# Kernel tuning notes

Measured on AMD Instinct MI355X. Metric: run time of the kernel, lower is better.

## Reference

```python
import jax, jax.numpy as jnp
import numpy as np
import math

B, S, D, H = 2, 2048, 1024, 16
DK = D // H


def setup_inputs() -> dict:
    key = jax.random.key(0)
    k1, k2, k3, k4, k5, k6 = jax.random.split(key, 6)
    scale = 1.0 / math.sqrt(D)
    return {
        "query": jax.random.normal(k1, (B, S, D), dtype=jnp.float32),
        "key": jax.random.normal(k2, (B, S, D), dtype=jnp.float32),
        "value": jax.random.normal(k3, (B, S, D), dtype=jnp.float32),
        "Wqkv": jax.random.normal(k4, (D, D), dtype=jnp.float32) * scale,
        "Wout": jax.random.normal(k5, (D, D), dtype=jnp.float32) * scale,
        "mask": jax.random.randint(k6, (B, 1, S, S), 0, 2, dtype=jnp.int32),
    }


def reference(query, key, value, Wqkv, Wout, mask):
    # Single shared QKV projection (same weight applied to q, k, v), no bias.
    q = query @ Wqkv.T
    k = key @ Wqkv.T
    v = value @ Wqkv.T
    # Faithful to the original: reshape (B, S, D) -> (B, H, S, DK) directly
    # (torch .reshape(n_batches, h, -1, d_k), NOT view+transpose).
    q = q.reshape(B, H, S, DK)
    k = k.reshape(B, H, S, DK)
    v = v.reshape(B, H, S, DK)
    scores = jnp.einsum("bhqd,bhkd->bhqk", q, k) / math.sqrt(DK)
    scores = jnp.where(mask == 0, jnp.float32(-1e9), scores)
    p_attn = jax.nn.softmax(scores, axis=-1)  # dropout is identity in eval
    x = jnp.einsum("bhqk,bhkd->bhqd", p_attn, v)  # [B,H,S,DK]
    x = x.transpose(0, 2, 1, 3).reshape(B, S, H * DK)
    return x @ Wout.T
```

## Files before the change

### kernel.cpp

```cpp
#include <hip/hip_runtime.h>
#include <stdint.h>


typedef __bf16 bf16;
typedef __bf16 bf16x8 __attribute__((ext_vector_type(8)));
typedef __bf16 bf16x4 __attribute__((ext_vector_type(4)));
typedef float f32x4 __attribute__((ext_vector_type(4)));

#define MFMA16(a, b, c) __builtin_amdgcn_mfma_f32_16x16x32_bf16((a), (b), (c), 0, 0, 0)
#define EXP2(x) __builtin_amdgcn_exp2f(x)

static constexpr int BATCH = 2;
static constexpr int SEQ = 2048;
static constexpr int DIM = 1024;
static constexpr int DK = 64;
static constexpr float QSCALE = 0.125f * 1.44269504088896340736f;

template <typename T>
struct Stripe;
template <>
struct Stripe<bf16> {
  uint4 v;
};
template <>
struct Stripe<float> {
  float4 a, b;
};

__device__ inline Stripe<bf16> load_stripe(const bf16* p) {
  Stripe<bf16> s;
  s.v = *(const uint4*)p;
  return s;
}
__device__ inline Stripe<float> load_stripe(const float* p) {
  Stripe<float> s;
  s.a = *(const float4*)p;
  s.b = *(const float4*)(p + 4);
  return s;
}
__device__ inline void store_stripe(bf16* d, const Stripe<bf16>& s) { *(uint4*)d = s.v; }
__device__ inline void store_stripe(bf16* d, const Stripe<float>& s) {
  bf16x8 v;
  v[0] = (bf16)s.a.x;
  v[1] = (bf16)s.a.y;
  v[2] = (bf16)s.a.z;
  v[3] = (bf16)s.a.w;
  v[4] = (bf16)s.b.x;
  v[5] = (bf16)s.b.y;
  v[6] = (bf16)s.b.z;
  v[7] = (bf16)s.b.w;
  *(bf16x8*)d = v;
}

__global__ __launch_bounds__(256) void mask_bits_kernel(const int* __restrict__ mask,
                                                        unsigned long long* __restrict__ bits) {
  int idx = blockIdx.x * 256 + threadIdx.x;
  int m = mask[idx];
  unsigned long long bal = __ballot(m != 0);
  if ((threadIdx.x & 63) == 0) bits[idx >> 6] = bal;
}

template <typename TA, typename TW, typename TC>
__global__ __launch_bounds__(256, 2) void gemm_bt(const TA* __restrict__ A0,
                                                  const TA* __restrict__ A1,
                                                  const TA* __restrict__ A2,
                                                  const TW* __restrict__ W,
                                                  TC* __restrict__ C0,
                                                  TC* __restrict__ C1,
                                                  TC* __restrict__ C2,
                                                  float scale0) {
  constexpr int K = 1024, N = 1024, LDA = 40;
  __shared__ bf16 As[128 * LDA];
  __shared__ bf16 Bs[128 * LDA];

  const TA* A = (blockIdx.z == 0) ? A0 : (blockIdx.z == 1) ? A1 : A2;
  TC* C = (blockIdx.z == 0) ? C0 : (blockIdx.z == 1) ? C1 : C2;
  const float sc = (blockIdx.z == 0) ? scale0 : 1.0f;

  const int tid = threadIdx.x;
  const int lane = tid & 63;
  const int wv = tid >> 6;
  const int wm = wv >> 1, wn = wv & 1;
  const int lrow = lane & 15, quad = lane >> 4;
  const int m0 = blockIdx.y * 128, n0 = blockIdx.x * 128;

  const f32x4 fz = {0.f, 0.f, 0.f, 0.f};
  f32x4 acc[4][4];
#pragma unroll
  for (int i = 0; i < 4; ++i)
#pragma unroll
    for (int j = 0; j < 4; ++j) acc[i][j] = fz;

  const int r0 = tid >> 2;
  const int c0 = (tid & 3) * 8;
  const TA* pa0 = A + (size_t)(m0 + r0) * K + c0;
  const TA* pa1 = A + (size_t)(m0 + r0 + 64) * K + c0;
  const TW* pb0 = W + (size_t)(n0 + r0) * K + c0;
  const TW* pb1 = W + (size_t)(n0 + r0 + 64) * K + c0;
  bf16* wa0 = &As[r0 * LDA + c0];
  bf16* wa1 = &As[(r0 + 64) * LDA + c0];
  bf16* wb0 = &Bs[r0 * LDA + c0];
  bf16* wb1 = &Bs[(r0 + 64) * LDA + c0];

  Stripe<TA> ra0 = load_stripe(pa0);
  Stripe<TA> ra1 = load_stripe(pa1);
  Stripe<TW> rb0 = load_stripe(pb0);
  Stripe<TW> rb1 = load_stripe(pb1);

  for (int k0 = 0; k0 < K; k0 += 32) {
    __syncthreads();
    store_stripe(wa0, ra0);
    store_stripe(wa1, ra1);
    store_stripe(wb0, rb0);
    store_stripe(wb1, rb1);
    __syncthreads();
    if (k0 + 32 < K) {
      ra0 = load_stripe(pa0 + k0 + 32);
      ra1 = load_stripe(pa1 + k0 + 32);
      rb0 = load_stripe(pb0 + k0 + 32);
      rb1 = load_stripe(pb1 + k0 + 32);
    }
    bf16x8 af[4], bfr[4];
#pragma unroll
    for (int mt = 0; mt < 4; ++mt)
      af[mt] = *(const bf16x8*)(&As[(wm * 64 + mt * 16 + lrow) * LDA + quad * 8]);
#pragma unroll
    for (int nt = 0; nt < 4; ++nt)
      bfr[nt] = *(const bf16x8*)(&Bs[(wn * 64 + nt * 16 + lrow) * LDA + quad * 8]);
#pragma unroll
    for (int mt = 0; mt < 4; ++mt)
#pragma unroll
      for (int nt = 0; nt < 4; ++nt) acc[mt][nt] = MFMA16(af[mt], bfr[nt], acc[mt][nt]);
  }

#pragma unroll
  for (int mt = 0; mt < 4; ++mt) {
    const int gm = m0 + wm * 64 + mt * 16 + quad * 4;
#pragma unroll
    for (int nt = 0; nt < 4; ++nt) {
      const int gn = n0 + wn * 64 + nt * 16 + lrow;
#pragma unroll
      for (int r = 0; r < 4; ++r) C[(size_t)(gm + r) * N + gn] = (TC)(acc[mt][nt][r] * sc);
    }
  }
}

__global__ __launch_bounds__(256, 2) void attn_kernel(const bf16* __restrict__ Qg,
                                                      const bf16* __restrict__ Kg,
                                                      const bf16* __restrict__ Vg,
                                                      const unsigned* __restrict__ bits,
                                                      bf16* __restrict__ Y) {
  constexpr int LQ = 72;
  __shared__ bf16 Qs[128 * LQ];
  __shared__ bf16 Ks[64 * LQ];
  __shared__ bf16 Vts[64 * LQ];
  __shared__ bf16 Ps[4][32 * LQ];
  __shared__ float Lrow[4][32];

  const int tid = threadIdx.x;
  const int lane = tid & 63;
  const int wv = tid >> 6;
  const int lrow = lane & 15, quad = lane >> 4;
  const int bh = blockIdx.y;
  const int b = bh >> 4, h = bh & 15;
  const int q0 = blockIdx.x * 128;

  const bf16* Qh = Qg + (size_t)bh * (SEQ * DK);
  const bf16* Kh = Kg + (size_t)bh * (SEQ * DK);
  const bf16* Vh = Vg + (size_t)bh * (SEQ * DK);

#pragma unroll
  for (int i = 0; i < 4; ++i) {
    int s = tid + i * 256;
    int row = s >> 3, c8 = (s & 7) * 8;
    *(uint4*)(&Qs[row * LQ + c8]) = *(const uint4*)(Qh + (size_t)(q0 + row) * DK + c8);
  }

  const int krow = tid >> 3;
  const int kc8 = (tid & 7) * 8;
  const bf16* pk0 = Kh + (size_t)krow * DK + kc8;
  const bf16* pk1 = Kh + (size_t)(krow + 32) * DK + kc8;
  const int vn2 = tid & 31;
  const int vk2b = tid >> 5;
  const bf16* pv0 = Vh + (size_t)(vk2b + 0) * 2 * DK + vn2 * 2;
  const bf16* pv1 = Vh + (size_t)(vk2b + 8) * 2 * DK + vn2 * 2;
  const bf16* pv2 = Vh + (size_t)(vk2b + 16) * 2 * DK + vn2 * 2;
  const bf16* pv3 = Vh + (size_t)(vk2b + 24) * 2 * DK + vn2 * 2;

  uint4 kr0, kr1;
  uint32_t va[4], vb[4];

  kr0 = *(const uint4*)(pk0);
  kr1 = *(const uint4*)(pk1);
  va[0] = *(const uint32_t*)(pv0);
  vb[0] = *(const uint32_t*)(pv0 + DK);
  va[1] = *(const uint32_t*)(pv1);
  vb[1] = *(const uint32_t*)(pv1 + DK);
  va[2] = *(const uint32_t*)(pv2);
  vb[2] = *(const uint32_t*)(pv2 + DK);
  va[3] = *(const uint32_t*)(pv3);
  vb[3] = *(const uint32_t*)(pv3 + DK);
  *(uint4*)(&Ks[krow * LQ + kc8]) = kr0;
  *(uint4*)(&Ks[(krow + 32) * LQ + kc8]) = kr1;
#pragma unroll
  for (int i = 0; i < 4; ++i) {
    uint32_t t0 = (va[i] & 0xffffu) | (vb[i] << 16);
    uint32_t t1 = (va[i] >> 16) | (vb[i] & 0xffff0000u);
    *(uint32_t*)(&Vts[(vn2 * 2) * LQ + (vk2b + i * 8) * 2]) = t0;
    *(uint32_t*)(&Vts[(vn2 * 2 + 1) * LQ + (vk2b + i * 8) * 2]) = t1;
  }
  __syncthreads();

  bf16x8 qf[2][2];
#pragma unroll
  for (int mt = 0; mt < 2; ++mt)
#pragma unroll
    for (int ks = 0; ks < 2; ++ks)
      qf[mt][ks] = *(const bf16x8*)(&Qs[(wv * 32 + mt * 16 + lrow) * LQ + ks * 32 + quad * 8]);
  __syncthreads();

  const f32x4 fz = {0.f, 0.f, 0.f, 0.f};
  f32x4 of_t[4][2];
#pragma unroll
  for (int i = 0; i < 4; ++i)
#pragma unroll
    for (int j = 0; j < 2; ++j) of_t[i][j] = fz;
  float lsum[2][4];
#pragma unroll
  for (int mt = 0; mt < 2; ++mt)
#pragma unroll
    for (int r = 0; r < 4; ++r) lsum[mt][r] = 0.f;

  const unsigned* bitrow = bits + (size_t)b * SEQ * (SEQ / 32);

  for (int kt = 0; kt < 32; ++kt) {
    const int cur = kt & 1;
    bf16* kb = cur ? Qs : Ks;
    bf16* vbuf = cur ? (Qs + 64 * LQ) : Vts;
    if (kt + 1 < 32) {
      const size_t adv = (size_t)(kt + 1) * 64 * DK;
      kr0 = *(const uint4*)(pk0 + adv);
      kr1 = *(const uint4*)(pk1 + adv);
      va[0] = *(const uint32_t*)(pv0 + adv);
      vb[0] = *(const uint32_t*)(pv0 + adv + DK);
      va[1] = *(const uint32_t*)(pv1 + adv);
      vb[1] = *(const uint32_t*)(pv1 + adv + DK);
      va[2] = *(const uint32_t*)(pv2 + adv);
      vb[2] = *(const uint32_t*)(pv2 + adv + DK);
      va[3] = *(const uint32_t*)(pv3 + adv);
      vb[3] = *(const uint32_t*)(pv3 + adv + DK);
    }
    uint2 mw[2][4];
#pragma unroll
    for (int mt = 0; mt < 2; ++mt)
#pragma unroll
      for (int r = 0; r < 4; ++r) {
        int row = q0 + wv * 32 + mt * 16 + quad * 4 + r;
        mw[mt][r] = *(const uint2*)(bitrow + (size_t)row * (SEQ / 32) + kt * 2);
      }

    f32x4 sf[2][4];
#pragma unroll
    for (int mt = 0; mt < 2; ++mt)
#pragma unroll
      for (int nt = 0; nt < 4; ++nt) sf[mt][nt] = fz;
#pragma unroll
    for (int ks = 0; ks < 2; ++ks) {
#pragma unroll
      for (int nt = 0; nt < 4; ++nt) {
        bf16x8 bk = *(const bf16x8*)(kb + (nt * 16 + lrow) * LQ + ks * 32 + quad * 8);
#pragma unroll
        for (int mt = 0; mt < 2; ++mt) sf[mt][nt] = MFMA16(qf[mt][ks], bk, sf[mt][nt]);
      }
    }

#pragma unroll
    for (int mt = 0; mt < 2; ++mt)
#pragma unroll
      for (int r = 0; r < 4; ++r) {
        uint32_t wx = mw[mt][r].x >> lrow;
        uint32_t wy = mw[mt][r].y >> lrow;
        float p0 = EXP2(sf[mt][0][r]);
        float p1 = EXP2(sf[mt][1][r]);
        float p2 = EXP2(sf[mt][2][r]);
        float p3 = EXP2(sf[mt][3][r]);
        p0 = (wx & 1u) ? p0 : 0.f;
        p1 = ((wx >> 16) & 1u) ? p1 : 0.f;
        p2 = (wy & 1u) ? p2 : 0.f;
        p3 = ((wy >> 16) & 1u) ? p3 : 0.f;
        lsum[mt][r] += (p0 + p1) + (p2 + p3);
        const int rbase = (mt * 16 + quad * 4 + r) * LQ + lrow;
        Ps[wv][rbase] = (bf16)p0;
        Ps[wv][rbase + 16] = (bf16)p1;
        Ps[wv][rbase + 32] = (bf16)p2;
        Ps[wv][rbase + 48] = (bf16)p3;
      }

#pragma unroll
    for (int ks = 0; ks < 2; ++ks) {
      bf16x8 avf[4], bpf[2];
#pragma unroll
      for (int dkt = 0; dkt < 4; ++dkt)
        avf[dkt] = *(const bf16x8*)(vbuf + (dkt * 16 + lrow) * LQ + ks * 32 + quad * 8);
#pragma unroll
      for (int rt = 0; rt < 2; ++rt)
        bpf[rt] = *(const bf16x8*)(&Ps[wv][(rt * 16 + lrow) * LQ + ks * 32 + quad * 8]);
#pragma unroll
      for (int dkt = 0; dkt < 4; ++dkt)
#pragma unroll
        for (int rt = 0; rt < 2; ++rt) of_t[dkt][rt] = MFMA16(avf[dkt], bpf[rt], of_t[dkt][rt]);
    }

    if (kt + 1 < 32) {
      bf16* kbn = cur ? Ks : Qs;
      bf16* vbn = cur ? Vts : (Qs + 64 * LQ);
      *(uint4*)(kbn + krow * LQ + kc8) = kr0;
      *(uint4*)(kbn + (krow + 32) * LQ + kc8) = kr1;
#pragma unroll
      for (int i = 0; i < 4; ++i) {
        uint32_t t0 = (va[i] & 0xffffu) | (vb[i] << 16);
        uint32_t t1 = (va[i] >> 16) | (vb[i] & 0xffff0000u);
        *(uint32_t*)(vbn + (vn2 * 2) * LQ + (vk2b + i * 8) * 2) = t0;
        *(uint32_t*)(vbn + (vn2 * 2 + 1) * LQ + (vk2b + i * 8) * 2) = t1;
      }
    }
    __syncthreads();
  }

#pragma unroll
  for (int mt = 0; mt < 2; ++mt)
#pragma unroll
    for (int r = 0; r < 4; ++r) {
      float v = lsum[mt][r];
      v += __shfl_xor(v, 1);
      v += __shfl_xor(v, 2);
      v += __shfl_xor(v, 4);
      v += __shfl_xor(v, 8);
      if (lrow == 0) Lrow[wv][mt * 16 + quad * 4 + r] = v;
    }
  __syncthreads();
  float linv[2];
#pragma unroll
  for (int rt = 0; rt < 2; ++rt) linv[rt] = 1.0f / fmaxf(Lrow[wv][rt * 16 + lrow], 1e-20f);

#pragma unroll
  for (int dkt = 0; dkt < 4; ++dkt)
#pragma unroll
    for (int rt = 0; rt < 2; ++rt) {
      bf16x4 o;
#pragma unroll
      for (int j = 0; j < 4; ++j) o[j] = (bf16)(of_t[dkt][rt][j] * linv[rt]);
      const int row = q0 + wv * 32 + rt * 16 + lrow;
      *(bf16x4*)(&Y[((size_t)b * SEQ + row) * DIM + h * 64 + dkt * 16 + quad * 4]) = o;
    }
}

extern "C" void kernel_launch(void* const* d_in, const int* in_sizes, int n_in,
                              void* d_out, int out_size, void* d_ws, size_t ws_size,
                              hipStream_t stream) {
  const float* query = (const float*)d_in[0];
  const float* key = (const float*)d_in[1];
  const float* value = (const float*)d_in[2];
  const float* Wqkv = (const float*)d_in[3];
  const float* Wout = (const float*)d_in[4];
  const int* mask = (const int*)d_in[5];
  float* out = (float*)d_out;

  char* ws = (char*)d_ws;
  bf16* q = (bf16*)(ws);
  bf16* k = (bf16*)(ws + 8388608);
  bf16* v = (bf16*)(ws + 16777216);
  bf16* y = (bf16*)(ws + 25165824);
  unsigned long long* bits64 = (unsigned long long*)(ws + 33554432);

  mask_bits_kernel<<<(BATCH * SEQ * SEQ) / 256, 256, 0, stream>>>(mask, bits64);

  gemm_bt<float, float, bf16>
      <<<dim3(8, 32, 3), 256, 0, stream>>>(query, key, value, Wqkv, q, k, v, QSCALE);

  attn_kernel<<<dim3(16, 32), 256, 0, stream>>>(q, k, v, (const unsigned*)bits64, y);

  gemm_bt<bf16, float, float>
      <<<dim3(8, 32, 1), 256, 0, stream>>>(y, y, y, Wout, out, out, out, 1.0f);
}
```

Baseline: 298.6 us.

## Transpose score MFMA to K·Q form and use 64-row tiles for output GEMM

The attention kernel now computes S^T with K as the A operand, so each lane holds four consecutive key columns for one query row. The P tile can then be written as packed bf16x4 stores, and the mask bits are loaded once per row rather than per register. Row sums become per-lane scalars reduced with two shuffles, which removes the LDS reduction and a block barrier. Separately, the output GEMM is templated to BM=64, doubling its grid to 512 blocks for better occupancy, at the cost of less B-tile reuse per block.

```diff
diff --git a/kernel.cpp b/kernel.cpp
--- a/kernel.cpp
+++ b/kernel.cpp
@@ -60,7 +60,7 @@
   if ((threadIdx.x & 63) == 0) bits[idx >> 6] = bal;
 }
 
-template <typename TA, typename TW, typename TC>
+template <int BM, typename TA, typename TW, typename TC>
 __global__ __launch_bounds__(256, 2) void gemm_bt(const TA* __restrict__ A0,
                                                   const TA* __restrict__ A1,
                                                   const TA* __restrict__ A2,
@@ -70,7 +70,8 @@
                                                   TC* __restrict__ C2,
                                                   float scale0) {
   constexpr int K = 1024, N = 1024, LDA = 40;
-  __shared__ bf16 As[128 * LDA];
+  constexpr int MT = BM / 32;
+  __shared__ bf16 As[BM * LDA];
   __shared__ bf16 Bs[128 * LDA];
 
   const TA* A = (blockIdx.z == 0) ? A0 : (blockIdx.z == 1) ? A1 : A2;
@@ -82,60 +83,62 @@
   const int wv = tid >> 6;
   const int wm = wv >> 1, wn = wv & 1;
   const int lrow = lane & 15, quad = lane >> 4;
-  const int m0 = blockIdx.y * 128, n0 = blockIdx.x * 128;
+  const int m0 = blockIdx.y * BM, n0 = blockIdx.x * 128;
 
   const f32x4 fz = {0.f, 0.f, 0.f, 0.f};
-  f32x4 acc[4][4];
-#pragma unroll
-  for (int i = 0; i < 4; ++i)
+  f32x4 acc[MT][4];
+#pragma unroll
+  for (int i = 0; i < MT; ++i)
 #pragma unroll
     for (int j = 0; j < 4; ++j) acc[i][j] = fz;
 
   const int r0 = tid >> 2;
   const int c0 = (tid & 3) * 8;
   const TA* pa0 = A + (size_t)(m0 + r0) * K + c0;
-  const TA* pa1 = A + (size_t)(m0 + r0 + 64) * K + c0;
+  const TA* pa1 = A + (size_t)(m0 + (r0 & (BM - 1) | 64 & (BM - 1)) ) * K + c0;
   const TW* pb0 = W + (size_t)(n0 + r0) * K + c0;
   const TW* pb1 = W + (size_t)(n0 + r0 + 64) * K + c0;
   bf16* wa0 = &As[r0 * LDA + c0];
-  bf16* wa1 = &As[(r0 + 64) * LDA + c0];
+  bf16* wa1 = &As[((r0 + 64) & (BM * 2 - 1)) * LDA + c0];
   bf16* wb0 = &Bs[r0 * LDA + c0];
   bf16* wb1 = &Bs[(r0 + 64) * LDA + c0];
+  if constexpr (BM == 128) pa1 = A + (size_t)(m0 + r0 + 64) * K + c0;
 
   Stripe<TA> ra0 = load_stripe(pa0);
-  Stripe<TA> ra1 = load_stripe(pa1);
+  Stripe<TA> ra1;
+  if constexpr (BM == 128) ra1 = load_stripe(pa1);
   Stripe<TW> rb0 = load_stripe(pb0);
   Stripe<TW> rb1 = load_stripe(pb1);
 
   for (int k0 = 0; k0 < K; k0 += 32) {
     __syncthreads();
     store_stripe(wa0, ra0);
-    store_stripe(wa1, ra1);
+    if constexpr (BM == 128) store_stripe(wa1, ra1);
     store_stripe(wb0, rb0);
     store_stripe(wb1, rb1);
     __syncthreads();
     if (k0 + 32 < K) {
       ra0 = load_stripe(pa0 + k0 + 32);
-      ra1 = load_stripe(pa1 + k0 + 32);
+      if constexpr (BM == 128) ra1 = load_stripe(pa1 + k0 + 32);
       rb0 = load_stripe(pb0 + k0 + 32);
       rb1 = load_stripe(pb1 + k0 + 32);
     }
-    bf16x8 af[4], bfr[4];
-#pragma unroll
-    for (int mt = 0; mt < 4; ++mt)
-      af[mt] = *(const bf16x8*)(&As[(wm * 64 + mt * 16 + lrow) * LDA + quad * 8]);
+    bf16x8 af[MT], bfr[4];
+#pragma unroll
+    for (int mt = 0; mt < MT; ++mt)
+      af[mt] = *(const bf16x8*)(&As[(wm * (BM / 2) + mt * 16 + lrow) * LDA + quad * 8]);
 #pragma unroll
     for (int nt = 0; nt < 4; ++nt)
       bfr[nt] = *(const bf16x8*)(&Bs[(wn * 64 + nt * 16 + lrow) * LDA + quad * 8]);
 #pragma unroll
-    for (int mt = 0; mt < 4; ++mt)
+    for (int mt = 0; mt < MT; ++mt)
 #pragma unroll
       for (int nt = 0; nt < 4; ++nt) acc[mt][nt] = MFMA16(af[mt], bfr[nt], acc[mt][nt]);
   }
 
 #pragma unroll
-  for (int mt = 0; mt < 4; ++mt) {
-    const int gm = m0 + wm * 64 + mt * 16 + quad * 4;
+  for (int mt = 0; mt < MT; ++mt) {
+    const int gm = m0 + wm * (BM / 2) + mt * 16 + quad * 4;
 #pragma unroll
     for (int nt = 0; nt < 4; ++nt) {
       const int gn = n0 + wn * 64 + nt * 16 + lrow;
@@ -155,7 +158,6 @@
   __shared__ bf16 Ks[64 * LQ];
   __shared__ bf16 Vts[64 * LQ];
   __shared__ bf16 Ps[4][32 * LQ];
-  __shared__ float Lrow[4][32];
 
   const int tid = threadIdx.x;
   const int lane = tid & 63;
@@ -213,10 +215,10 @@
 
   bf16x8 qf[2][2];
 #pragma unroll
-  for (int mt = 0; mt < 2; ++mt)
+  for (int nt = 0; nt < 2; ++nt)
 #pragma unroll
     for (int ks = 0; ks < 2; ++ks)
-      qf[mt][ks] = *(const bf16x8*)(&Qs[(wv * 32 + mt * 16 + lrow) * LQ + ks * 32 + quad * 8]);
+      qf[nt][ks] = *(const bf16x8*)(&Qs[(wv * 32 + nt * 16 + lrow) * LQ + ks * 32 + quad * 8]);
   __syncthreads();
 
   const f32x4 fz = {0.f, 0.f, 0.f, 0.f};
@@ -225,11 +227,7 @@
   for (int i = 0; i < 4; ++i)
 #pragma unroll
     for (int j = 0; j < 2; ++j) of_t[i][j] = fz;
-  float lsum[2][4];
-#pragma unroll
-  for (int mt = 0; mt < 2; ++mt)
-#pragma unroll
-    for (int r = 0; r < 4; ++r) lsum[mt][r] = 0.f;
+  float lsum[2] = {0.f, 0.f};
 
   const unsigned* bitrow = bits + (size_t)b * SEQ * (SEQ / 32);
 
@@ -250,51 +248,49 @@
       va[3] = *(const uint32_t*)(pv3 + adv);
       vb[3] = *(const uint32_t*)(pv3 + adv + DK);
     }
-    uint2 mw[2][4];
-#pragma unroll
-    for (int mt = 0; mt < 2; ++mt)
-#pragma unroll
-      for (int r = 0; r < 4; ++r) {
-        int row = q0 + wv * 32 + mt * 16 + quad * 4 + r;
-        mw[mt][r] = *(const uint2*)(bitrow + (size_t)row * (SEQ / 32) + kt * 2);
+    uint2 mwn[2];
+#pragma unroll
+    for (int nt = 0; nt < 2; ++nt) {
+      int row = q0 + wv * 32 + nt * 16 + lrow;
+      mwn[nt] = *(const uint2*)(bitrow + (size_t)row * (SEQ / 32) + kt * 2);
+    }
+
+    f32x4 st[4][2];
+#pragma unroll
+    for (int mt = 0; mt < 4; ++mt)
+#pragma unroll
+      for (int nt = 0; nt < 2; ++nt) st[mt][nt] = fz;
+#pragma unroll
+    for (int ks = 0; ks < 2; ++ks) {
+#pragma unroll
+      for (int mt = 0; mt < 4; ++mt) {
+        bf16x8 kfv = *(const bf16x8*)(kb + (mt * 16 + lrow) * LQ + ks * 32 + quad * 8);
+#pragma unroll
+        for (int nt = 0; nt < 2; ++nt) st[mt][nt] = MFMA16(kfv, qf[nt][ks], st[mt][nt]);
       }
-
-    f32x4 sf[2][4];
-#pragma unroll
-    for (int mt = 0; mt < 2; ++mt)
-#pragma unroll
-      for (int nt = 0; nt < 4; ++nt) sf[mt][nt] = fz;
-#pragma unroll
-    for (int ks = 0; ks < 2; ++ks) {
-#pragma unroll
-      for (int nt = 0; nt < 4; ++nt) {
-        bf16x8 bk = *(const bf16x8*)(kb + (nt * 16 + lrow) * LQ + ks * 32 + quad * 8);
-#pragma unroll
-        for (int mt = 0; mt < 2; ++mt) sf[mt][nt] = MFMA16(qf[mt][ks], bk, sf[mt][nt]);
+    }
+
+#pragma unroll
+    for (int nt = 0; nt < 2; ++nt) {
+      uint32_t ux = mwn[nt].x >> (quad * 4);
+      uint32_t uy = mwn[nt].y >> (quad * 4);
+      float psum = 0.f;
+#pragma unroll
+      for (int mt = 0; mt < 4; ++mt) {
+        uint32_t u = (mt & 2) ? uy : ux;
+        int sh = (mt & 1) << 4;
+        bf16x4 pk;
+#pragma unroll
+        for (int r = 0; r < 4; ++r) {
+          float p = EXP2(st[mt][nt][r]);
+          p = ((u >> (sh + r)) & 1u) ? p : 0.f;
+          psum += p;
+          pk[r] = (bf16)p;
+        }
+        *(bf16x4*)(&Ps[wv][(nt * 16 + lrow) * LQ + mt * 16 + quad * 4]) = pk;
       }
-    }
-
-#pragma unroll
-    for (int mt = 0; mt < 2; ++mt)
-#pragma unroll
-      for (int r = 0; r < 4; ++r) {
-        uint32_t wx = mw[mt][r].x >> lrow;
-        uint32_t wy = mw[mt][r].y >> lrow;
-        float p0 = EXP2(sf[mt][0][r]);
-        float p1 = EXP2(sf[mt][1][r]);
-        float p2 = EXP2(sf[mt][2][r]);
-        float p3 = EXP2(sf[mt][3][r]);
-        p0 = (wx & 1u) ? p0 : 0.f;
-        p1 = ((wx >> 16) & 1u) ? p1 : 0.f;
-        p2 = (wy & 1u) ? p2 : 0.f;
-        p3 = ((wy >> 16) & 1u) ? p3 : 0.f;
-        lsum[mt][r] += (p0 + p1) + (p2 + p3);
-        const int rbase = (mt * 16 + quad * 4 + r) * LQ + lrow;
-        Ps[wv][rbase] = (bf16)p0;
-        Ps[wv][rbase + 16] = (bf16)p1;
-        Ps[wv][rbase + 32] = (bf16)p2;
-        Ps[wv][rbase + 48] = (bf16)p3;
-      }
+      lsum[nt] += psum;
+    }
 
 #pragma unroll
     for (int ks = 0; ks < 2; ++ks) {
@@ -327,21 +323,14 @@
     __syncthreads();
   }
 
-#pragma unroll
-  for (int mt = 0; mt < 2; ++mt)
-#pragma unroll
-    for (int r = 0; r < 4; ++r) {
-      float v = lsum[mt][r];
-      v += __shfl_xor(v, 1);
-      v += __shfl_xor(v, 2);
-      v += __shfl_xor(v, 4);
-      v += __shfl_xor(v, 8);
-      if (lrow == 0) Lrow[wv][mt * 16 + quad * 4 + r] = v;
-    }
-  __syncthreads();
   float linv[2];
 #pragma unroll
-  for (int rt = 0; rt < 2; ++rt) linv[rt] = 1.0f / fmaxf(Lrow[wv][rt * 16 + lrow], 1e-20f);
+  for (int nt = 0; nt < 2; ++nt) {
+    float v = lsum[nt];
+    v += __shfl_xor(v, 16);
+    v += __shfl_xor(v, 32);
+    linv[nt] = 1.0f / fmaxf(v, 1e-20f);
+  }
 
 #pragma unroll
   for (int dkt = 0; dkt < 4; ++dkt)
@@ -375,11 +364,11 @@
 
   mask_bits_kernel<<<(BATCH * SEQ * SEQ) / 256, 256, 0, stream>>>(mask, bits64);
 
-  gemm_bt<float, float, bf16>
+  gemm_bt<128, float, float, bf16>
       <<<dim3(8, 32, 3), 256, 0, stream>>>(query, key, value, Wqkv, q, k, v, QSCALE);
 
   attn_kernel<<<dim3(16, 32), 256, 0, stream>>>(q, k, v, (const unsigned*)bits64, y);
 
-  gemm_bt<bf16, float, float>
-      <<<dim3(8, 32, 1), 256, 0, stream>>>(y, y, y, Wout, out, out, out, 1.0f);
-}
+  gemm_bt<64, bf16, float, float>
+      <<<dim3(8, 64, 1), 256, 0, stream>>>(y, y, y, Wout, out, out, out, 1.0f);
+}
```

Result: faster. 283.4 us (-5.1%).
